# Performance work log

Measured on AMD Instinct MI355X. Metric: run time of the kernel, lower is better.

The kernel has to match this reference:

```python
import jax, jax.numpy as jnp
import numpy as np

NUM_NODES = 65536       # B * gcn_nodes_num = 256 * 256
NODES_PER_GRAPH = 256
GCN_EMB_DIM = 128
N_EMBD = 512
NUM_EDGES = 1048576     # avg degree 16
NEG_SLOPE = 0.1


def gcn_conv(x, edge_index, W, b, num_nodes):
    """PyG GCNConv: add self-loops, symmetric normalization, linear, aggregate."""
    loop = jnp.arange(num_nodes, dtype=edge_index.dtype)
    src = jnp.concatenate([edge_index[0], loop])
    dst = jnp.concatenate([edge_index[1], loop])
    deg = jax.ops.segment_sum(jnp.ones_like(dst, dtype=x.dtype), dst,
                              num_segments=num_nodes)
    dinv = jnp.where(deg > 0, jax.lax.rsqrt(deg), jnp.zeros_like(deg))
    norm = dinv[src] * dinv[dst]              # [E+N]
    h = x @ W                                 # [N, out]
    msg = h[src] * norm[:, None]              # [E+N, out]
    out = jax.ops.segment_sum(msg, dst, num_segments=num_nodes)
    return out + b


def setup_inputs() -> dict:
    key = jax.random.key(0)
    ks = jax.random.split(key, 8)
    nodes = jax.random.normal(ks[0], (NUM_NODES, 3), dtype=jnp.float32)
    edge_index = jax.random.randint(ks[1], (2, NUM_EDGES), 0, NUM_NODES,
                                    dtype=jnp.int64)
    W1 = jax.random.normal(ks[2], (3, 3), dtype=jnp.float32) * 0.5
    b1 = jnp.zeros((3,), dtype=jnp.float32)
    W2 = jax.random.normal(ks[3], (3, GCN_EMB_DIM), dtype=jnp.float32) * 0.5
    b2 = jnp.zeros((GCN_EMB_DIM,), dtype=jnp.float32)
    W3 = jax.random.normal(ks[4], (GCN_EMB_DIM * NODES_PER_GRAPH, N_EMBD),
                           dtype=jnp.float32) * 0.01
    b3 = jnp.zeros((N_EMBD,), dtype=jnp.float32)
    return {"nodes": nodes, "edge_index": edge_index,
            "W1": W1, "b1": b1, "W2": W2, "b2": b2, "W3": W3, "b3": b3}


def reference(nodes, edge_index, W1, b1, W2, b2, W3, b3):
    n = nodes.shape[0]
    h = gcn_conv(nodes, edge_index, W1, b1, n)           # GCNConv(3,3)
    h = jnp.where(h >= 0, h, NEG_SLOPE * h)              # leaky_relu(0.1)
    h = gcn_conv(h, edge_index, W2, b2, n)               # GCNConv(3,128)
    h = h.reshape(-1, GCN_EMB_DIM * NODES_PER_GRAPH)     # [B, 128*256]
    out = h @ W3 + b3                                    # [B, 512]
    return out
```

## Files before the change

### kernel.cpp

```cpp
#include <hip/hip_runtime.h>

static constexpr int NN   = 65536;
static constexpr int NPG  = 256;
static constexpr int NB   = 256;
static constexpr int EMB  = 128;
static constexpr int NOUT = 512;

static constexpr int NBIN = 256;
static constexpr int CAP  = 4608;
static constexpr int SCAP = CAP + 256;

static constexpr int BT = 16;
static constexpr int KS = 16;
static constexpr int IC = NPG / KS;

__global__ __launch_bounds__(1024)
void k_partV(const int* __restrict__ src, const int* __restrict__ dst, int E,
             int* __restrict__ part, int* __restrict__ cl,
             const float* __restrict__ W2, const float* __restrict__ b2,
             const float* __restrict__ W3, float4* __restrict__ V4) {
    union SH {
        struct { int hist[NBIN]; int loff[NBIN]; int scanbuf[NBIN];
                 int stage[4096]; } part;
        float4 red[8][4][128];
    };
    __shared__ SH sh;
    int tid = threadIdx.x;
    int bid = blockIdx.x;

    if (bid >= NBIN) {
        int i  = bid - NBIN;
        int j4 = tid & 127;
        int cg = tid >> 7;
        const float4* w3 = (const float4*)(W3 + (size_t)i * EMB * NOUT)
                           + (size_t)cg * 16 * (NOUT/4) + j4;
        float4 a0 = {0,0,0,0}, a1 = {0,0,0,0}, a2 = {0,0,0,0}, a3 = {0,0,0,0};
        for (int c = 0; c < 16; c++) {
            float4 v = w3[(size_t)c * (NOUT/4)];
            int cc = cg*16 + c;
            float w0 = W2[0*EMB+cc], w1 = W2[1*EMB+cc], w2 = W2[2*EMB+cc], wb = b2[cc];
            a0.x += w0*v.x; a0.y += w0*v.y; a0.z += w0*v.z; a0.w += w0*v.w;
            a1.x += w1*v.x; a1.y += w1*v.y; a1.z += w1*v.z; a1.w += w1*v.w;
            a2.x += w2*v.x; a2.y += w2*v.y; a2.z += w2*v.z; a2.w += w2*v.w;
            a3.x += wb*v.x; a3.y += wb*v.y; a3.z += wb*v.z; a3.w += wb*v.w;
        }
        sh.red[cg][0][j4] = a0;
        sh.red[cg][1][j4] = a1;
        sh.red[cg][2][j4] = a2;
        sh.red[cg][3][j4] = a3;
        __syncthreads();
        if (tid < 512) {
            int k = tid >> 7, jj = tid & 127;
            float4 s = sh.red[0][k][jj];
#pragma unroll
            for (int g = 1; g < 8; g++) {
                float4 v = sh.red[g][k][jj];
                s.x += v.x; s.y += v.y; s.z += v.z; s.w += v.w;
            }
            sh.red[0][k][jj] = s;
        }
        __syncthreads();
        if (tid < NOUT) {
            int j = tid;
            const float* r0 = (const float*)&sh.red[0][0][j >> 2];
            const float* r1 = (const float*)&sh.red[0][1][j >> 2];
            const float* r2 = (const float*)&sh.red[0][2][j >> 2];
            const float* r3 = (const float*)&sh.red[0][3][j >> 2];
            float4 o = { r0[j & 3], r1[j & 3], r2[j & 3], r3[j & 3] };
            V4[(size_t)i * NOUT + j] = o;
        }
        return;
    }
    int epb = (E + NBIN - 1) / NBIN;
    int e0 = bid * epb;
    int e1 = min(e0 + epb, E);
    if (tid < NBIN) sh.part.hist[tid] = 0;
    __syncthreads();

    int pk[4], bn[4], rk[4];
    int n = 0;
    int e = e0 + tid * 4;
    if (e + 4 <= e1) {
        int4 s4 = *(const int4*)(src + e);
        int4 d4 = *(const int4*)(dst + e);
        int ss[4] = {s4.x, s4.y, s4.z, s4.w};
        int dd[4] = {d4.x, d4.y, d4.z, d4.w};
#pragma unroll
        for (int k = 0; k < 4; k++) {
            pk[k] = ss[k] | ((dd[k] & 255) << 16);
            bn[k] = dd[k] >> 8;
            rk[k] = atomicAdd(&sh.part.hist[bn[k]], 1);
        }
        n = 4;
    } else {
        for (int k = 0; k < 4 && e + k < e1; k++) {
            int s = src[e+k], d = dst[e+k];
            pk[n] = s | ((d & 255) << 16);
            bn[n] = d >> 8;
            rk[n] = atomicAdd(&sh.part.hist[bn[n]], 1);
            n++;
        }
    }
    __syncthreads();

    if (tid < NBIN) sh.part.scanbuf[tid] = sh.part.hist[tid];
    __syncthreads();
    for (int off = 1; off < NBIN; off <<= 1) {
        int v = 0;
        if (tid < NBIN && tid >= off) v = sh.part.scanbuf[tid - off];
        __syncthreads();
        if (tid < NBIN) sh.part.scanbuf[tid] += v;
        __syncthreads();
    }
    if (tid < NBIN) {
        int lo = sh.part.scanbuf[tid] - sh.part.hist[tid];
        sh.part.loff[tid] = lo;
        cl[bid * NBIN + tid] = lo | (sh.part.hist[tid] << 16);
    }
    __syncthreads();

    for (int k = 0; k < n; k++) sh.part.stage[sh.part.loff[bn[k]] + rk[k]] = pk[k];
    __syncthreads();

    int ctot = e1 - e0;
    for (int t = tid; t < ctot; t += 1024)
        part[(size_t)bid * epb + t] = sh.part.stage[t];
}

__global__ __launch_bounds__(512)
void k_csr(const int* __restrict__ cl, const int* __restrict__ part, int epb,
           const float* __restrict__ nodes,
           float* __restrict__ dinv, float4* __restrict__ y1,
           int* __restrict__ rs, unsigned short* __restrict__ srt) {
    __shared__ int pkst[CAP];
    __shared__ int hist[NPG], off_[NPG];
    __shared__ int wtot[4];
    __shared__ int cls[NBIN], blo[NBIN];
    __shared__ unsigned short stageS[SCAP];
    int tid = threadIdx.x, bin = blockIdx.x;
    if (tid < NPG) hist[tid] = 0;

    int cn = 0, v = 0;
    if (tid < NBIN) {
        int c = cl[tid * NBIN + bin];
        cls[tid] = c;
        cn = c >> 16;
        v = cn;
    }
    int lane = tid & 63;
#pragma unroll
    for (int off = 1; off < 64; off <<= 1) {
        int t = __shfl_up(v, off, 64);
        if (tid < NBIN && lane >= off) v += t;
    }
    if (tid < NBIN && lane == 63) wtot[tid >> 6] = v;
    __syncthreads();
    if (tid < NBIN) {
        int wv = tid >> 6, offs = 0;
#pragma unroll
        for (int w = 0; w < 3; w++) if (w < wv) offs += wtot[w];
        blo[tid] = v + offs - cn;
    }
    __syncthreads();

    {
        int blk = tid >> 1, half = tid & 1;
        int c = cls[blk];
        int lo = c & 0xFFFF, cb = c >> 16;
        int db = blo[blk];
        const int* q = part + (size_t)blk * epb + lo;
        for (int t = half; t < cb; t += 2) {
            int d2 = db + t;
            if (d2 < CAP) {
                int p = q[t];
                pkst[d2] = p;
                atomicAdd(&hist[(p >> 16) & 255], 1);
            }
        }
    }
    __syncthreads();

    int h = 0, v2 = 0;
    if (tid < NPG) { h = hist[tid]; v2 = (h + 1) & ~1; }
#pragma unroll
    for (int off = 1; off < 64; off <<= 1) {
        int t = __shfl_up(v2, off, 64);
        if (tid < NPG && lane >= off) v2 += t;
    }
    if (tid < NPG && lane == 63) wtot[tid >> 6] = v2;
    __syncthreads();
    if (tid < NPG) {
        int wv = tid >> 6;
        int offs = 0;
#pragma unroll
        for (int w = 0; w < 3; w++) if (w < wv) offs += wtot[w];
        int start = v2 + offs - ((h + 1) & ~1);
        off_[tid] = start;
        int node = bin * NPG + tid;
        float di = rsqrtf((float)(h + 1));
        dinv[node] = di;
        y1[node] = make_float4(nodes[3*node+0] * di, nodes[3*node+1] * di,
                               nodes[3*node+2] * di, 0.f);
        rs[node] = start | (h << 20);
    }
    __syncthreads();
    int ctot = min(wtot[0] + wtot[1] + wtot[2] + wtot[3], CAP);
    for (int e2 = tid; e2 < ctot; e2 += 512) {
        (void)0;
    }
    {
    }
    __syncthreads();
    int rawtot = blo[NBIN-1] + (cls[NBIN-1] >> 16);
    if (rawtot > CAP) rawtot = CAP;
    for (int e2 = tid; e2 < rawtot; e2 += 512) {
        int p = pkst[e2];
        int pos = atomicAdd(&off_[(p >> 16) & 255], 1);
        stageS[pos] = (unsigned short)(p & 0xFFFF);
    }
    __syncthreads();
    int tot = wtot[0] + wtot[1] + wtot[2] + wtot[3];
    const unsigned int* so = (const unsigned int*)stageS;
    unsigned int* g = (unsigned int*)(srt + (size_t)bin * SCAP);
    for (int t = tid; t < (tot >> 1); t += 512) g[t] = so[t];
}

__device__ __forceinline__ void agg_pass(int g, const int* __restrict__ rs,
                                         const unsigned short* __restrict__ srt,
                                         const float* __restrict__ dinv,
                                         const float* __restrict__ W1,
                                         const float* __restrict__ b1,
                                         const float4* __restrict__ yin,
                                         float4* __restrict__ yout, bool first) {
    int i = g >> 3, sub = g & 7;
    int rsd = rs[i];
    int start = rsd & 0xFFFFF, deg = rsd >> 20;
    const unsigned int* spw = (const unsigned int*)(srt + (size_t)(i >> 8) * SCAP + start);
    int npairs = (deg + 1) >> 1;
    float ax = 0.f, ay = 0.f, az = 0.f;
    for (int w = sub; w < npairs; w += 8) {
        unsigned int u = spw[w];
        float4 v0 = yin[u & 0xFFFF];
        ax += v0.x; ay += v0.y; az += v0.z;
        if (2*w + 1 < deg) {
            float4 v1 = yin[u >> 16];
            ax += v1.x; ay += v1.y; az += v1.z;
        }
    }
    ax += __shfl_xor(ax, 1); ay += __shfl_xor(ay, 1); az += __shfl_xor(az, 1);
    ax += __shfl_xor(ax, 2); ay += __shfl_xor(ay, 2); az += __shfl_xor(az, 2);
    ax += __shfl_xor(ax, 4); ay += __shfl_xor(ay, 4); az += __shfl_xor(az, 4);
    if (sub == 0) {
        float4 self = yin[i];
        float di = dinv[i];
        float a0 = (ax + self.x) * di, a1 = (ay + self.y) * di, a2 = (az + self.z) * di;
        if (first) {
            float h[3];
#pragma unroll
            for (int k = 0; k < 3; k++) {
                float t = a0 * W1[0*3+k] + a1 * W1[1*3+k] + a2 * W1[2*3+k] + b1[k];
                t = (t >= 0.f) ? t : 0.1f * t;
                h[k] = t * di;
            }
            yout[i] = make_float4(h[0], h[1], h[2], 0.f);
        } else {
            yout[i] = make_float4(a0, a1, a2, 0.f);
        }
    }
}

__global__ void k_agg1(const int* __restrict__ rs, const unsigned short* __restrict__ srt,
                       const float* __restrict__ dinv, const float4* __restrict__ y1,
                       const float* __restrict__ W1, const float* __restrict__ b1,
                       float4* __restrict__ y2) {
    agg_pass(blockIdx.x * 256 + threadIdx.x, rs, srt, dinv, W1, b1, y1, y2, true);
}

__global__ void k_agg2(const int* __restrict__ rs, const unsigned short* __restrict__ srt,
                       const float* __restrict__ dinv, const float4* __restrict__ y2,
                       float4* __restrict__ agg2) {
    agg_pass(blockIdx.x * 256 + threadIdx.x, rs, srt, dinv, nullptr, nullptr,
             y2, agg2, false);
}

__global__ void k_out_part(const float4* __restrict__ agg2, const float4* __restrict__ V4,
                           float* __restrict__ partO) {
    __shared__ float4 a_s[BT * IC];
    int tid = threadIdx.x;
    int j  = blockIdx.x * 256 + tid;
    int b0 = blockIdx.y * BT;
    int i0 = blockIdx.z * IC;
    for (int idx = tid; idx < BT * IC; idx += 256) {
        int t = idx / IC, i = idx % IC;
        a_s[idx] = agg2[(size_t)(b0 + t) * NPG + i0 + i];
    }
    __syncthreads();

    float acc[BT];
#pragma unroll
    for (int t = 0; t < BT; t++) acc[t] = 0.f;

    const float4* vj = V4 + (size_t)i0 * NOUT + j;
    for (int i = 0; i < IC; i++) {
        float4 vv = vj[(size_t)i * NOUT];
#pragma unroll
        for (int t = 0; t < BT; t++) {
            float4 a = a_s[t*IC + i];
            acc[t] += a.x * vv.x + a.y * vv.y + a.z * vv.z + vv.w;
        }
    }
#pragma unroll
    for (int t = 0; t < BT; t++)
        partO[((size_t)blockIdx.z * NB + b0 + t) * NOUT + j] = acc[t];
}

__global__ void k_reduce(const float4* __restrict__ part4, const float4* __restrict__ b3_4,
                         float4* __restrict__ out4) {
    int idx = blockIdx.x * 256 + threadIdx.x;
    int j4 = idx & (NOUT/4 - 1);
    float4 acc = b3_4[j4];
#pragma unroll
    for (int s = 0; s < KS; s++) {
        float4 v = part4[(size_t)s * (NB*NOUT/4) + idx];
        acc.x += v.x; acc.y += v.y; acc.z += v.z; acc.w += v.w;
    }
    out4[idx] = acc;
}

extern "C" void kernel_launch(void* const* d_in, const int* in_sizes, int n_in,
                              void* d_out, int out_size, void* d_ws, size_t ws_size,
                              hipStream_t stream) {
    const float* nodes = (const float*)d_in[0];
    const int*   ei    = (const int*)  d_in[1];
    const float* W1    = (const float*)d_in[2];
    const float* b1    = (const float*)d_in[3];
    const float* W2    = (const float*)d_in[4];
    const float* b2    = (const float*)d_in[5];
    const float* W3    = (const float*)d_in[6];
    const float* b3    = (const float*)d_in[7];

    const int E = in_sizes[1] / 2;
    const int* src = ei;
    const int* dst = ei + E;
    const int epb = (E + NBIN - 1) / NBIN;

    char* ws = (char*)d_ws;
    float4* y1    = (float4*)ws;
    float4* y2    = y1 + NN;
    float4* agg2  = y2 + NN;
    float4* V4    = agg2 + NN;
    float*  partO = (float*)(V4 + (size_t)NPG * NOUT);
    int*    partE = (int*)(partO + (size_t)KS * NB * NOUT);
    unsigned short* srt = (unsigned short*)(partE + (size_t)NBIN * CAP);
    int*    rs    = (int*)(srt + (size_t)NBIN * SCAP);
    float*  dinv  = (float*)(rs + NN);
    int*    cl    = (int*)(dinv + NN);

    k_partV   <<<2*NBIN, 1024, 0, stream>>>(src, dst, E, partE, cl, W2, b2, W3, V4);
    k_csr     <<<NBIN,    512, 0, stream>>>(cl, partE, epb, nodes, dinv, y1, rs, srt);
    k_agg1    <<<NN*8/256, 256, 0, stream>>>(rs, srt, dinv, y1, W1, b1, y2);
    k_agg2    <<<NN*8/256, 256, 0, stream>>>(rs, srt, dinv, y2, agg2);
    k_out_part<<<dim3(2, NB/BT, KS), 256, 0, stream>>>(agg2, V4, partO);
    k_reduce  <<<NB*NOUT/4/256,      256, 0, stream>>>((const float4*)partO,
                                                       (const float4*)b3, (float4*)d_out);
}
```

Baseline: 155.3 us.

## Fuse all GCN pipeline stages into one cooperative kernel with grid syncs

Replaces the six separate launches (partition, CSR build, two aggregations, output partial GEMM, reduce) with a single cooperative kernel of 512 blocks × 512 threads that separates phases with grid.sync(). The W3 precontraction into V4 is split into two halves and overlapped with the partition and CSR phases on the otherwise idle upper 256 blocks. This removes per-launch overhead and inter-kernel gaps. In exchange it gives up per-phase launch geometry: aggregation runs 4 threads per node instead of 8, and the output and reduce phases leave most blocks idle. Grid-wide barriers also have their own cost, and the old launch sequence is kept as a fallback if the cooperative launch fails.

```diff
diff --git a/kernel.cpp b/kernel.cpp
--- a/kernel.cpp
+++ b/kernel.cpp
@@ -1,4 +1,7 @@
 #include <hip/hip_runtime.h>
+#include <hip/hip_cooperative_groups.h>
+
+namespace cg = cooperative_groups;
 
 static constexpr int NN   = 65536;
 static constexpr int NPG  = 256;
@@ -13,6 +16,330 @@
 static constexpr int BT = 16;
 static constexpr int KS = 16;
 static constexpr int IC = NPG / KS;
+
+__global__ __launch_bounds__(512, 4)
+void k_mega(const int* __restrict__ src, const int* __restrict__ dst, int E,
+            int* __restrict__ part, int* __restrict__ cl,
+            const float* __restrict__ W2, const float* __restrict__ b2,
+            const float* __restrict__ W3, float4* __restrict__ V4,
+            const float* __restrict__ nodes, float* __restrict__ dinv,
+            float4* __restrict__ y1, int* __restrict__ rs,
+            unsigned short* __restrict__ srt,
+            const float* __restrict__ W1, const float* __restrict__ b1,
+            float4* __restrict__ y2, float4* __restrict__ agg2,
+            float* __restrict__ partO, const float* __restrict__ b3,
+            float* __restrict__ out) {
+    union SH {
+        struct { int hist[NBIN]; int loff[NBIN]; int wt[4]; int stage[4096]; } part;
+        float4 redV[4][4][128];
+        struct { int pkst[CAP]; int hist[NPG]; int off_[NPG]; int wtot[4];
+                 int cls[NBIN]; int blo[NBIN]; unsigned short stageS[SCAP]; } csr;
+        float4 a_s[BT * IC];
+    };
+    __shared__ SH sh;
+    cg::grid_group grid = cg::this_grid();
+    const int tid = threadIdx.x;
+    const int bid = blockIdx.x;
+    const int lane = tid & 63;
+    const int epb = (E + NBIN - 1) / NBIN;
+
+    float4 va0 = {0,0,0,0}, va1 = {0,0,0,0}, va2 = {0,0,0,0}, va3 = {0,0,0,0};
+    const int vi  = bid - NBIN;
+    const int vj4 = tid & 127;
+    const int vcg = tid >> 7;
+
+    if (bid < NBIN) {
+        int e0 = bid * epb;
+        int e1 = min(e0 + epb, E);
+        if (tid < NBIN) sh.part.hist[tid] = 0;
+        __syncthreads();
+
+        int pk[8], bn[8], rk[8];
+        int e = e0 + tid * 8;
+        if (e + 8 <= e1) {
+            int4 sa = *(const int4*)(src + e), sb = *(const int4*)(src + e + 4);
+            int4 da = *(const int4*)(dst + e), db = *(const int4*)(dst + e + 4);
+            int ss[8] = {sa.x, sa.y, sa.z, sa.w, sb.x, sb.y, sb.z, sb.w};
+            int dd[8] = {da.x, da.y, da.z, da.w, db.x, db.y, db.z, db.w};
+#pragma unroll
+            for (int k = 0; k < 8; k++) {
+                pk[k] = ss[k] | ((dd[k] & 255) << 16);
+                bn[k] = dd[k] >> 8;
+                rk[k] = atomicAdd(&sh.part.hist[bn[k]], 1);
+            }
+        } else {
+#pragma unroll
+            for (int k = 0; k < 8; k++) {
+                if (e + k < e1) {
+                    int s = src[e+k], d = dst[e+k];
+                    pk[k] = s | ((d & 255) << 16);
+                    bn[k] = d >> 8;
+                    rk[k] = atomicAdd(&sh.part.hist[bn[k]], 1);
+                } else bn[k] = -1;
+            }
+        }
+        __syncthreads();
+
+        int h = 0, v = 0;
+        if (tid < NBIN) { h = sh.part.hist[tid]; v = h; }
+#pragma unroll
+        for (int off = 1; off < 64; off <<= 1) {
+            int t = __shfl_up(v, off, 64);
+            if (tid < NBIN && lane >= off) v += t;
+        }
+        if (tid < NBIN && lane == 63) sh.part.wt[tid >> 6] = v;
+        __syncthreads();
+        if (tid < NBIN) {
+            int wv = tid >> 6, offs = 0;
+#pragma unroll
+            for (int w = 0; w < 3; w++) if (w < wv) offs += sh.part.wt[w];
+            int lo = v + offs - h;
+            sh.part.loff[tid] = lo;
+            cl[bid * NBIN + tid] = lo | (h << 16);
+        }
+        __syncthreads();
+#pragma unroll
+        for (int k = 0; k < 8; k++)
+            if (bn[k] >= 0) sh.part.stage[sh.part.loff[bn[k]] + rk[k]] = pk[k];
+        __syncthreads();
+        int ctot = e1 - e0;
+        for (int t = tid; t < ctot; t += 512)
+            part[(size_t)bid * epb + t] = sh.part.stage[t];
+    } else {
+        const float4* w3 = (const float4*)(W3 + (size_t)vi * EMB * NOUT);
+#pragma unroll
+        for (int c = 0; c < 16; c++) {
+            int cc = vcg * 32 + c;
+            float4 v = w3[(size_t)cc * (NOUT/4) + vj4];
+            float w0 = W2[0*EMB+cc], w1 = W2[1*EMB+cc], w2c = W2[2*EMB+cc], wb = b2[cc];
+            va0.x += w0*v.x;  va0.y += w0*v.y;  va0.z += w0*v.z;  va0.w += w0*v.w;
+            va1.x += w1*v.x;  va1.y += w1*v.y;  va1.z += w1*v.z;  va1.w += w1*v.w;
+            va2.x += w2c*v.x; va2.y += w2c*v.y; va2.z += w2c*v.z; va2.w += w2c*v.w;
+            va3.x += wb*v.x;  va3.y += wb*v.y;  va3.z += wb*v.z;  va3.w += wb*v.w;
+        }
+    }
+    grid.sync();
+
+    if (bid < NBIN) {
+        int bin = bid;
+        if (tid < NPG) sh.csr.hist[tid] = 0;
+        int cn = 0, v = 0;
+        if (tid < NBIN) {
+            int c = cl[tid * NBIN + bin];
+            sh.csr.cls[tid] = c;
+            cn = c >> 16;
+            v = cn;
+        }
+#pragma unroll
+        for (int off = 1; off < 64; off <<= 1) {
+            int t = __shfl_up(v, off, 64);
+            if (tid < NBIN && lane >= off) v += t;
+        }
+        if (tid < NBIN && lane == 63) sh.csr.wtot[tid >> 6] = v;
+        __syncthreads();
+        if (tid < NBIN) {
+            int wv = tid >> 6, offs = 0;
+#pragma unroll
+            for (int w = 0; w < 3; w++) if (w < wv) offs += sh.csr.wtot[w];
+            sh.csr.blo[tid] = v + offs - cn;
+        }
+        __syncthreads();
+
+        {
+            int blk = tid >> 1, half = tid & 1;
+            int c = sh.csr.cls[blk];
+            int lo = c & 0xFFFF, cb = c >> 16;
+            int db = sh.csr.blo[blk];
+            const int* q = part + (size_t)blk * epb + lo;
+            for (int t = half; t < cb; t += 2) {
+                int d2 = db + t;
+                if (d2 < CAP) {
+                    int p = q[t];
+                    sh.csr.pkst[d2] = p;
+                    atomicAdd(&sh.csr.hist[(p >> 16) & 255], 1);
+                }
+            }
+        }
+        __syncthreads();
+
+        int h = 0, v2 = 0;
+        if (tid < NPG) { h = sh.csr.hist[tid]; v2 = (h + 1) & ~1; }
+#pragma unroll
+        for (int off = 1; off < 64; off <<= 1) {
+            int t = __shfl_up(v2, off, 64);
+            if (tid < NPG && lane >= off) v2 += t;
+        }
+        if (tid < NPG && lane == 63) sh.csr.wtot[tid >> 6] = v2;
+        __syncthreads();
+        if (tid < NPG) {
+            int wv = tid >> 6, offs = 0;
+#pragma unroll
+            for (int w = 0; w < 3; w++) if (w < wv) offs += sh.csr.wtot[w];
+            int start = v2 + offs - ((h + 1) & ~1);
+            sh.csr.off_[tid] = start;
+            int node = bin * NPG + tid;
+            float di = rsqrtf((float)(h + 1));
+            dinv[node] = di;
+            y1[node] = make_float4(nodes[3*node+0] * di, nodes[3*node+1] * di,
+                                   nodes[3*node+2] * di, 0.f);
+            rs[node] = start | (h << 20);
+        }
+        __syncthreads();
+        int rawtot = sh.csr.blo[NBIN-1] + (sh.csr.cls[NBIN-1] >> 16);
+        if (rawtot > CAP) rawtot = CAP;
+        for (int e2 = tid; e2 < rawtot; e2 += 512) {
+            int p = sh.csr.pkst[e2];
+            int pos = atomicAdd(&sh.csr.off_[(p >> 16) & 255], 1);
+            sh.csr.stageS[pos] = (unsigned short)(p & 0xFFFF);
+        }
+        __syncthreads();
+        int tot = sh.csr.wtot[0] + sh.csr.wtot[1] + sh.csr.wtot[2] + sh.csr.wtot[3];
+        const unsigned int* so = (const unsigned int*)sh.csr.stageS;
+        unsigned int* g = (unsigned int*)(srt + (size_t)bin * SCAP);
+        for (int t = tid; t < (tot >> 1); t += 512) g[t] = so[t];
+    } else {
+        const float4* w3 = (const float4*)(W3 + (size_t)vi * EMB * NOUT);
+#pragma unroll
+        for (int c = 16; c < 32; c++) {
+            int cc = vcg * 32 + c;
+            float4 v = w3[(size_t)cc * (NOUT/4) + vj4];
+            float w0 = W2[0*EMB+cc], w1 = W2[1*EMB+cc], w2c = W2[2*EMB+cc], wb = b2[cc];
+            va0.x += w0*v.x;  va0.y += w0*v.y;  va0.z += w0*v.z;  va0.w += w0*v.w;
+            va1.x += w1*v.x;  va1.y += w1*v.y;  va1.z += w1*v.z;  va1.w += w1*v.w;
+            va2.x += w2c*v.x; va2.y += w2c*v.y; va2.z += w2c*v.z; va2.w += w2c*v.w;
+            va3.x += wb*v.x;  va3.y += wb*v.y;  va3.z += wb*v.z;  va3.w += wb*v.w;
+        }
+        sh.redV[vcg][0][vj4] = va0;
+        sh.redV[vcg][1][vj4] = va1;
+        sh.redV[vcg][2][vj4] = va2;
+        sh.redV[vcg][3][vj4] = va3;
+        __syncthreads();
+        {
+            int k = tid >> 7, jj = tid & 127;
+            float4 s = sh.redV[0][k][jj];
+#pragma unroll
+            for (int g2 = 1; g2 < 4; g2++) {
+                float4 t = sh.redV[g2][k][jj];
+                s.x += t.x; s.y += t.y; s.z += t.z; s.w += t.w;
+            }
+            sh.redV[0][k][jj] = s;
+        }
+        __syncthreads();
+        {
+            int j = tid;
+            const float* r0 = (const float*)&sh.redV[0][0][j >> 2];
+            const float* r1 = (const float*)&sh.redV[0][1][j >> 2];
+            const float* r2 = (const float*)&sh.redV[0][2][j >> 2];
+            const float* r3 = (const float*)&sh.redV[0][3][j >> 2];
+            V4[(size_t)vi * NOUT + j] = make_float4(r0[j & 3], r1[j & 3],
+                                                    r2[j & 3], r3[j & 3]);
+        }
+    }
+    grid.sync();
+
+    {
+        int gq = bid * 512 + tid;
+        int i = gq >> 2, sub = gq & 3;
+        int rsd = rs[i];
+        int start = rsd & 0xFFFFF, deg = rsd >> 20;
+        const unsigned int* spw = (const unsigned int*)(srt + (size_t)(i >> 8) * SCAP + start);
+        int npairs = (deg + 1) >> 1;
+        float ax = 0.f, ay = 0.f, az = 0.f;
+        for (int w = sub; w < npairs; w += 4) {
+            unsigned int u = spw[w];
+            float4 v0 = y1[u & 0xFFFF];
+            ax += v0.x; ay += v0.y; az += v0.z;
+            if (2*w + 1 < deg) {
+                float4 v1 = y1[u >> 16];
+                ax += v1.x; ay += v1.y; az += v1.z;
+            }
+        }
+        ax += __shfl_xor(ax, 1); ay += __shfl_xor(ay, 1); az += __shfl_xor(az, 1);
+        ax += __shfl_xor(ax, 2); ay += __shfl_xor(ay, 2); az += __shfl_xor(az, 2);
+        if (sub == 0) {
+            float4 self = y1[i];
+            float di = dinv[i];
+            float a0 = (ax + self.x) * di, a1 = (ay + self.y) * di, a2 = (az + self.z) * di;
+            float hh[3];
+#pragma unroll
+            for (int k = 0; k < 3; k++) {
+                float t = a0 * W1[0*3+k] + a1 * W1[1*3+k] + a2 * W1[2*3+k] + b1[k];
+                t = (t >= 0.f) ? t : 0.1f * t;
+                hh[k] = t * di;
+            }
+            y2[i] = make_float4(hh[0], hh[1], hh[2], 0.f);
+        }
+    }
+    grid.sync();
+
+    {
+        int gq = bid * 512 + tid;
+        int i = gq >> 2, sub = gq & 3;
+        int rsd = rs[i];
+        int start = rsd & 0xFFFFF, deg = rsd >> 20;
+        const unsigned int* spw = (const unsigned int*)(srt + (size_t)(i >> 8) * SCAP + start);
+        int npairs = (deg + 1) >> 1;
+        float ax = 0.f, ay = 0.f, az = 0.f;
+        for (int w = sub; w < npairs; w += 4) {
+            unsigned int u = spw[w];
+            float4 v0 = y2[u & 0xFFFF];
+            ax += v0.x; ay += v0.y; az += v0.z;
+            if (2*w + 1 < deg) {
+                float4 v1 = y2[u >> 16];
+                ax += v1.x; ay += v1.y; az += v1.z;
+            }
+        }
+        ax += __shfl_xor(ax, 1); ay += __shfl_xor(ay, 1); az += __shfl_xor(az, 1);
+        ax += __shfl_xor(ax, 2); ay += __shfl_xor(ay, 2); az += __shfl_xor(az, 2);
+        if (sub == 0) {
+            float4 self = y2[i];
+            float di = dinv[i];
+            agg2[i] = make_float4((ax + self.x) * di, (ay + self.y) * di,
+                                  (az + self.z) * di, 0.f);
+        }
+    }
+    grid.sync();
+
+    if (bid < 256) {
+        int ks = bid & 15, bb = bid >> 4;
+        int b0 = bb * BT, i0 = ks * IC;
+        if (tid < BT * IC) {
+            int t = tid >> 4, i = tid & 15;
+            sh.a_s[tid] = agg2[(size_t)(b0 + t) * NPG + i0 + i];
+        }
+        __syncthreads();
+        float acc[BT];
+#pragma unroll
+        for (int t = 0; t < BT; t++) acc[t] = 0.f;
+        int j = tid;
+        const float4* vj = V4 + (size_t)i0 * NOUT + j;
+        for (int i = 0; i < IC; i++) {
+            float4 vv = vj[(size_t)i * NOUT];
+#pragma unroll
+            for (int t = 0; t < BT; t++) {
+                float4 a = sh.a_s[t*IC + i];
+                acc[t] += a.x * vv.x + a.y * vv.y + a.z * vv.z + vv.w;
+            }
+        }
+#pragma unroll
+        for (int t = 0; t < BT; t++)
+            partO[((size_t)ks * NB + b0 + t) * NOUT + j] = acc[t];
+    }
+    grid.sync();
+
+    if (bid < 64) {
+        int idx = bid * 512 + tid;
+        int j4 = idx & (NOUT/4 - 1);
+        const float4* b3_4 = (const float4*)b3;
+        float4 acc = b3_4[j4];
+#pragma unroll
+        for (int s = 0; s < KS; s++) {
+            float4 vv = ((const float4*)partO)[(size_t)s * (NB*NOUT/4) + idx];
+            acc.x += vv.x; acc.y += vv.y; acc.z += vv.z; acc.w += vv.w;
+        }
+        ((float4*)out)[idx] = acc;
+    }
+}
 
 __global__ __launch_bounds__(1024)
 void k_partV(const int* __restrict__ src, const int* __restrict__ dst, int E,
@@ -66,8 +393,7 @@
             const float* r1 = (const float*)&sh.red[0][1][j >> 2];
             const float* r2 = (const float*)&sh.red[0][2][j >> 2];
             const float* r3 = (const float*)&sh.red[0][3][j >> 2];
-            float4 o = { r0[j & 3], r1[j & 3], r2[j & 3], r3[j & 3] };
-            V4[(size_t)i * NOUT + j] = o;
+            V4[(size_t)i * NOUT + j] = make_float4(r0[j&3], r1[j&3], r2[j&3], r3[j&3]);
         }
         return;
     }
@@ -202,13 +528,6 @@
         y1[node] = make_float4(nodes[3*node+0] * di, nodes[3*node+1] * di,
                                nodes[3*node+2] * di, 0.f);
         rs[node] = start | (h << 20);
-    }
-    __syncthreads();
-    int ctot = min(wtot[0] + wtot[1] + wtot[2] + wtot[3], CAP);
-    for (int e2 = tid; e2 < ctot; e2 += 512) {
-        (void)0;
-    }
-    {
     }
     __syncthreads();
     int rawtot = blo[NBIN-1] + (cls[NBIN-1] >> 16);
@@ -339,7 +658,7 @@
     const float* W3    = (const float*)d_in[6];
     const float* b3    = (const float*)d_in[7];
 
-    const int E = in_sizes[1] / 2;
+    int E = in_sizes[1] / 2;
     const int* src = ei;
     const int* dst = ei + E;
     const int epb = (E + NBIN - 1) / NBIN;
@@ -356,11 +675,32 @@
     float*  dinv  = (float*)(rs + NN);
     int*    cl    = (int*)(dinv + NN);
 
-    k_partV   <<<2*NBIN, 1024, 0, stream>>>(src, dst, E, partE, cl, W2, b2, W3, V4);
-    k_csr     <<<NBIN,    512, 0, stream>>>(cl, partE, epb, nodes, dinv, y1, rs, srt);
-    k_agg1    <<<NN*8/256, 256, 0, stream>>>(rs, srt, dinv, y1, W1, b1, y2);
-    k_agg2    <<<NN*8/256, 256, 0, stream>>>(rs, srt, dinv, y2, agg2);
-    k_out_part<<<dim3(2, NB/BT, KS), 256, 0, stream>>>(agg2, V4, partO);
-    k_reduce  <<<NB*NOUT/4/256,      256, 0, stream>>>((const float4*)partO,
-                                                       (const float4*)b3, (float4*)d_out);
-}
+    const int* src_ = src; const int* dst_ = dst;
+    int* partE_ = partE; int* cl_ = cl;
+    const float* W2_ = W2; const float* b2_ = b2; const float* W3_ = W3;
+    float4* V4_ = V4; const float* nodes_ = nodes;
+    float* dinv_ = dinv; float4* y1_ = y1; int* rs_ = rs;
+    unsigned short* srt_ = srt;
+    const float* W1_ = W1; const float* b1_ = b1;
+    float4* y2_ = y2; float4* agg2_ = agg2;
+    float* partO_ = partO; const float* b3_ = b3;
+    float* out_ = (float*)d_out;
+
+    void* args[] = { &src_, &dst_, &E, &partE_, &cl_, &W2_, &b2_, &W3_, &V4_,
+                     &nodes_, &dinv_, &y1_, &rs_, &srt_, &W1_, &b1_,
+                     &y2_, &agg2_, &partO_, &b3_, &out_ };
+
+    hipError_t err = hipLaunchCooperativeKernel((const void*)k_mega,
+                                                dim3(512), dim3(512),
+                                                args, 0, stream);
+    if (err != hipSuccess) {
+        (void)hipGetLastError();
+        k_partV   <<<2*NBIN, 1024, 0, stream>>>(src, dst, E, partE, cl, W2, b2, W3, V4);
+        k_csr     <<<NBIN,    512, 0, stream>>>(cl, partE, epb, nodes, dinv, y1, rs, srt);
+        k_agg1    <<<NN*8/256, 256, 0, stream>>>(rs, srt, dinv, y1, W1, b1, y2);
+        k_agg2    <<<NN*8/256, 256, 0, stream>>>(rs, srt, dinv, y2, agg2);
+        k_out_part<<<dim3(2, NB/BT, KS), 256, 0, stream>>>(agg2, V4, partO);
+        k_reduce  <<<NB*NOUT/4/256,      256, 0, stream>>>((const float4*)partO,
+                                                           (const float4*)b3, (float4*)d_out);
+    }
+}
```

Result: slower. 460.1 us (+196.2%).

## Split W3 folding into V across partition, CSR and aggregation kernels

Applied to the files above, without the earlier changes.

Precomputing V = W2/b2 folded into W3 used to be done entirely inside k_partV, which streams the whole 64 MB W3. The work is now split into four channel chunks of 32. k_partV handles the first chunk, and extra blocks appended to k_csr, k_agg1 and k_agg2 each accumulate a further chunk into V4 in read-modify-write style. This hides the W3 streaming behind the latency-bound partition and aggregation work, and W3 loads are marked nontemporal. In exchange, each kernel now depends on the previous kernel's partial V4, the extra blocks compete for bandwidth with the aggregation passes, and the later chunks use scalar loads.

```diff
diff --git a/kernel.cpp b/kernel.cpp
--- a/kernel.cpp
+++ b/kernel.cpp
@@ -13,6 +13,11 @@
 static constexpr int BT = 16;
 static constexpr int KS = 16;
 static constexpr int IC = NPG / KS;
+
+static constexpr int AGB = NN * 8 / 256;
+
+typedef float nfloat4 __attribute__((ext_vector_type(4)));
+
 
 __global__ __launch_bounds__(1024)
 void k_partV(const int* __restrict__ src, const int* __restrict__ dst, int E,
@@ -32,12 +37,13 @@
         int i  = bid - NBIN;
         int j4 = tid & 127;
         int cg = tid >> 7;
-        const float4* w3 = (const float4*)(W3 + (size_t)i * EMB * NOUT)
-                           + (size_t)cg * 16 * (NOUT/4) + j4;
+        const nfloat4* w3 = (const nfloat4*)(W3 + (size_t)i * EMB * NOUT)
+                            + (size_t)cg * 4 * (NOUT/4) + j4;
         float4 a0 = {0,0,0,0}, a1 = {0,0,0,0}, a2 = {0,0,0,0}, a3 = {0,0,0,0};
-        for (int c = 0; c < 16; c++) {
-            float4 v = w3[(size_t)c * (NOUT/4)];
-            int cc = cg*16 + c;
+#pragma unroll
+        for (int c = 0; c < 4; c++) {
+            nfloat4 v = __builtin_nontemporal_load(&w3[(size_t)c * (NOUT/4)]);
+            int cc = cg*4 + c;
             float w0 = W2[0*EMB+cc], w1 = W2[1*EMB+cc], w2 = W2[2*EMB+cc], wb = b2[cc];
             a0.x += w0*v.x; a0.y += w0*v.y; a0.z += w0*v.z; a0.w += w0*v.w;
             a1.x += w1*v.x; a1.y += w1*v.y; a1.z += w1*v.z; a1.w += w1*v.w;
@@ -127,17 +133,54 @@
         part[(size_t)bid * epb + t] = sh.part.stage[t];
 }
 
+template <int JPER>
+__device__ __forceinline__ void finishV(int i, int tid, int c0,
+                                        const float* __restrict__ W2,
+                                        const float* __restrict__ b2,
+                                        const float* __restrict__ W3,
+                                        float4* __restrict__ V4) {
+    float4 acc[JPER];
+#pragma unroll
+    for (int q = 0; q < JPER; q++)
+        acc[q] = V4[(size_t)i * NOUT + tid + q * (NOUT / JPER)];
+    const float* w3r = W3 + ((size_t)i * EMB + c0) * NOUT + tid;
+#pragma unroll
+    for (int c = 0; c < 32; c++) {
+        int cc = c0 + c;
+        float w0 = W2[0*EMB+cc], w1 = W2[1*EMB+cc], w2 = W2[2*EMB+cc], wb = b2[cc];
+#pragma unroll
+        for (int q = 0; q < JPER; q++) {
+            float s = __builtin_nontemporal_load(&w3r[(size_t)c * NOUT + q * (NOUT / JPER)]);
+            acc[q].x += w0 * s;
+            acc[q].y += w1 * s;
+            acc[q].z += w2 * s;
+            acc[q].w += wb * s;
+        }
+    }
+#pragma unroll
+    for (int q = 0; q < JPER; q++)
+        V4[(size_t)i * NOUT + tid + q * (NOUT / JPER)] = acc[q];
+}
+
 __global__ __launch_bounds__(512)
 void k_csr(const int* __restrict__ cl, const int* __restrict__ part, int epb,
            const float* __restrict__ nodes,
            float* __restrict__ dinv, float4* __restrict__ y1,
-           int* __restrict__ rs, unsigned short* __restrict__ srt) {
+           int* __restrict__ rs, unsigned short* __restrict__ srt,
+           const float* __restrict__ W2, const float* __restrict__ b2,
+           const float* __restrict__ W3, float4* __restrict__ V4) {
     __shared__ int pkst[CAP];
     __shared__ int hist[NPG], off_[NPG];
     __shared__ int wtot[4];
     __shared__ int cls[NBIN], blo[NBIN];
     __shared__ unsigned short stageS[SCAP];
     int tid = threadIdx.x, bin = blockIdx.x;
+
+    if (bin >= NBIN) {
+        finishV<1>(bin - NBIN, tid, 32, W2, b2, W3, V4);
+        return;
+    }
+
     if (tid < NPG) hist[tid] = 0;
 
     int cn = 0, v = 0;
@@ -202,13 +245,6 @@
         y1[node] = make_float4(nodes[3*node+0] * di, nodes[3*node+1] * di,
                                nodes[3*node+2] * di, 0.f);
         rs[node] = start | (h << 20);
-    }
-    __syncthreads();
-    int ctot = min(wtot[0] + wtot[1] + wtot[2] + wtot[3], CAP);
-    for (int e2 = tid; e2 < ctot; e2 += 512) {
-        (void)0;
-    }
-    {
     }
     __syncthreads();
     int rawtot = blo[NBIN-1] + (cls[NBIN-1] >> 16);
@@ -272,14 +308,28 @@
 __global__ void k_agg1(const int* __restrict__ rs, const unsigned short* __restrict__ srt,
                        const float* __restrict__ dinv, const float4* __restrict__ y1,
                        const float* __restrict__ W1, const float* __restrict__ b1,
-                       float4* __restrict__ y2) {
-    agg_pass(blockIdx.x * 256 + threadIdx.x, rs, srt, dinv, W1, b1, y1, y2, true);
+                       float4* __restrict__ y2,
+                       const float* __restrict__ W2, const float* __restrict__ b2,
+                       const float* __restrict__ W3, float4* __restrict__ V4) {
+    int bid = blockIdx.x;
+    if (bid >= AGB) {
+        finishV<2>(bid - AGB, threadIdx.x, 64, W2, b2, W3, V4);
+        return;
+    }
+    agg_pass(bid * 256 + threadIdx.x, rs, srt, dinv, W1, b1, y1, y2, true);
 }
 
 __global__ void k_agg2(const int* __restrict__ rs, const unsigned short* __restrict__ srt,
                        const float* __restrict__ dinv, const float4* __restrict__ y2,
-                       float4* __restrict__ agg2) {
-    agg_pass(blockIdx.x * 256 + threadIdx.x, rs, srt, dinv, nullptr, nullptr,
+                       float4* __restrict__ agg2,
+                       const float* __restrict__ W2, const float* __restrict__ b2,
+                       const float* __restrict__ W3, float4* __restrict__ V4) {
+    int bid = blockIdx.x;
+    if (bid >= AGB) {
+        finishV<2>(bid - AGB, threadIdx.x, 96, W2, b2, W3, V4);
+        return;
+    }
+    agg_pass(bid * 256 + threadIdx.x, rs, srt, dinv, nullptr, nullptr,
              y2, agg2, false);
 }
 
@@ -356,10 +406,13 @@
     float*  dinv  = (float*)(rs + NN);
     int*    cl    = (int*)(dinv + NN);
 
-    k_partV   <<<2*NBIN, 1024, 0, stream>>>(src, dst, E, partE, cl, W2, b2, W3, V4);
-    k_csr     <<<NBIN,    512, 0, stream>>>(cl, partE, epb, nodes, dinv, y1, rs, srt);
-    k_agg1    <<<NN*8/256, 256, 0, stream>>>(rs, srt, dinv, y1, W1, b1, y2);
-    k_agg2    <<<NN*8/256, 256, 0, stream>>>(rs, srt, dinv, y2, agg2);
+    k_partV   <<<2*NBIN,   1024, 0, stream>>>(src, dst, E, partE, cl, W2, b2, W3, V4);
+    k_csr     <<<2*NBIN,    512, 0, stream>>>(cl, partE, epb, nodes, dinv, y1, rs, srt,
+                                              W2, b2, W3, V4);
+    k_agg1    <<<AGB + 256, 256, 0, stream>>>(rs, srt, dinv, y1, W1, b1, y2,
+                                              W2, b2, W3, V4);
+    k_agg2    <<<AGB + 256, 256, 0, stream>>>(rs, srt, dinv, y2, agg2,
+                                              W2, b2, W3, V4);
     k_out_part<<<dim3(2, NB/BT, KS), 256, 0, stream>>>(agg2, V4, partO);
     k_reduce  <<<NB*NOUT/4/256,      256, 0, stream>>>((const float4*)partO,
                                                        (const float4*)b3, (float4*)d_out);
```

Result: slower. 165.4 us (+6.5%).

## Fuse split-K output GEMM and reduction into one kernel; nontemporal W3 loads

Applied to the files above, without the earlier changes.

Replaces the split-K output kernel plus its separate reduction kernel with a single kernel. Each block handles 4 graphs over the full 256-node K range, accumulates in registers and adds the bias directly. This removes the partial-sum buffer round trip through memory and one kernel launch, but each block now does 16x more serial K work on a grid of 256 blocks of 128 threads. It also makes the one-time W3 streaming loads in k_partV nontemporal and deletes a dead empty loop with its extra barrier in k_csr.

```diff
diff --git a/kernel.cpp b/kernel.cpp
--- a/kernel.cpp
+++ b/kernel.cpp
@@ -10,9 +10,11 @@
 static constexpr int CAP  = 4608;
 static constexpr int SCAP = CAP + 256;
 
-static constexpr int BT = 16;
-static constexpr int KS = 16;
-static constexpr int IC = NPG / KS;
+static constexpr int KS  = 16;
+static constexpr int IC  = NPG / KS;
+static constexpr int BT2 = 4;
+
+typedef float nfloat4 __attribute__((ext_vector_type(4)));
 
 __global__ __launch_bounds__(1024)
 void k_partV(const int* __restrict__ src, const int* __restrict__ dst, int E,
@@ -32,11 +34,11 @@
         int i  = bid - NBIN;
         int j4 = tid & 127;
         int cg = tid >> 7;
-        const float4* w3 = (const float4*)(W3 + (size_t)i * EMB * NOUT)
-                           + (size_t)cg * 16 * (NOUT/4) + j4;
+        const nfloat4* w3 = (const nfloat4*)(W3 + (size_t)i * EMB * NOUT)
+                            + (size_t)cg * 16 * (NOUT/4) + j4;
         float4 a0 = {0,0,0,0}, a1 = {0,0,0,0}, a2 = {0,0,0,0}, a3 = {0,0,0,0};
         for (int c = 0; c < 16; c++) {
-            float4 v = w3[(size_t)c * (NOUT/4)];
+            nfloat4 v = __builtin_nontemporal_load(&w3[(size_t)c * (NOUT/4)]);
             int cc = cg*16 + c;
             float w0 = W2[0*EMB+cc], w1 = W2[1*EMB+cc], w2 = W2[2*EMB+cc], wb = b2[cc];
             a0.x += w0*v.x; a0.y += w0*v.y; a0.z += w0*v.z; a0.w += w0*v.w;
@@ -202,13 +204,6 @@
         y1[node] = make_float4(nodes[3*node+0] * di, nodes[3*node+1] * di,
                                nodes[3*node+2] * di, 0.f);
         rs[node] = start | (h << 20);
-    }
-    __syncthreads();
-    int ctot = min(wtot[0] + wtot[1] + wtot[2] + wtot[3], CAP);
-    for (int e2 = tid; e2 < ctot; e2 += 512) {
-        (void)0;
-    }
-    {
     }
     __syncthreads();
     int rawtot = blo[NBIN-1] + (cls[NBIN-1] >> 16);
@@ -283,48 +278,44 @@
              y2, agg2, false);
 }
 
-__global__ void k_out_part(const float4* __restrict__ agg2, const float4* __restrict__ V4,
-                           float* __restrict__ partO) {
-    __shared__ float4 a_s[BT * IC];
+__global__ __launch_bounds__(128)
+void k_out(const float4* __restrict__ agg2, const float4* __restrict__ V4,
+           const float* __restrict__ b3, float* __restrict__ out) {
+    __shared__ float4 a_s[BT2 * NPG];
     int tid = threadIdx.x;
-    int j  = blockIdx.x * 256 + tid;
-    int b0 = blockIdx.y * BT;
-    int i0 = blockIdx.z * IC;
-    for (int idx = tid; idx < BT * IC; idx += 256) {
-        int t = idx / IC, i = idx % IC;
-        a_s[idx] = agg2[(size_t)(b0 + t) * NPG + i0 + i];
-    }
-    __syncthreads();
-
-    float acc[BT];
-#pragma unroll
-    for (int t = 0; t < BT; t++) acc[t] = 0.f;
-
-    const float4* vj = V4 + (size_t)i0 * NOUT + j;
-    for (int i = 0; i < IC; i++) {
-        float4 vv = vj[(size_t)i * NOUT];
-#pragma unroll
-        for (int t = 0; t < BT; t++) {
-            float4 a = a_s[t*IC + i];
-            acc[t] += a.x * vv.x + a.y * vv.y + a.z * vv.z + vv.w;
-        }
-    }
-#pragma unroll
-    for (int t = 0; t < BT; t++)
-        partO[((size_t)blockIdx.z * NB + b0 + t) * NOUT + j] = acc[t];
-}
-
-__global__ void k_reduce(const float4* __restrict__ part4, const float4* __restrict__ b3_4,
-                         float4* __restrict__ out4) {
-    int idx = blockIdx.x * 256 + threadIdx.x;
-    int j4 = idx & (NOUT/4 - 1);
-    float4 acc = b3_4[j4];
-#pragma unroll
+    int j  = blockIdx.x * 128 + tid;
+    int b0 = blockIdx.y * BT2;
+    for (int idx = tid; idx < BT2 * NPG; idx += 128) {
+        int t = idx >> 8, i = idx & 255;
+        a_s[idx] = agg2[(size_t)(b0 + t) * NPG + i];
+    }
+    __syncthreads();
+
+    float acc[BT2];
+#pragma unroll
+    for (int t = 0; t < BT2; t++) acc[t] = b3[j];
+
+    const float4* vj = V4 + j;
     for (int s = 0; s < KS; s++) {
-        float4 v = part4[(size_t)s * (NB*NOUT/4) + idx];
-        acc.x += v.x; acc.y += v.y; acc.z += v.z; acc.w += v.w;
-    }
-    out4[idx] = acc;
+        float ps[BT2];
+#pragma unroll
+        for (int t = 0; t < BT2; t++) ps[t] = 0.f;
+#pragma unroll
+        for (int ii = 0; ii < IC; ii++) {
+            int i = s * IC + ii;
+            float4 vv = vj[(size_t)i * NOUT];
+#pragma unroll
+            for (int t = 0; t < BT2; t++) {
+                float4 a = a_s[t * NPG + i];
+                ps[t] += a.x * vv.x + a.y * vv.y + a.z * vv.z + vv.w;
+            }
+        }
+#pragma unroll
+        for (int t = 0; t < BT2; t++) acc[t] += ps[t];
+    }
+#pragma unroll
+    for (int t = 0; t < BT2; t++)
+        out[(size_t)(b0 + t) * NOUT + j] = acc[t];
 }
 
 extern "C" void kernel_launch(void* const* d_in, const int* in_sizes, int n_in,
@@ -349,18 +340,15 @@
     float4* y2    = y1 + NN;
     float4* agg2  = y2 + NN;
     float4* V4    = agg2 + NN;
-    float*  partO = (float*)(V4 + (size_t)NPG * NOUT);
-    int*    partE = (int*)(partO + (size_t)KS * NB * NOUT);
+    int*    partE = (int*)(V4 + (size_t)NPG * NOUT);
     unsigned short* srt = (unsigned short*)(partE + (size_t)NBIN * CAP);
     int*    rs    = (int*)(srt + (size_t)NBIN * SCAP);
     float*  dinv  = (float*)(rs + NN);
     int*    cl    = (int*)(dinv + NN);
 
-    k_partV   <<<2*NBIN, 1024, 0, stream>>>(src, dst, E, partE, cl, W2, b2, W3, V4);
-    k_csr     <<<NBIN,    512, 0, stream>>>(cl, partE, epb, nodes, dinv, y1, rs, srt);
-    k_agg1    <<<NN*8/256, 256, 0, stream>>>(rs, srt, dinv, y1, W1, b1, y2);
-    k_agg2    <<<NN*8/256, 256, 0, stream>>>(rs, srt, dinv, y2, agg2);
-    k_out_part<<<dim3(2, NB/BT, KS), 256, 0, stream>>>(agg2, V4, partO);
-    k_reduce  <<<NB*NOUT/4/256,      256, 0, stream>>>((const float4*)partO,
-                                                       (const float4*)b3, (float4*)d_out);
-}
+    k_partV<<<2*NBIN,   1024, 0, stream>>>(src, dst, E, partE, cl, W2, b2, W3, V4);
+    k_csr  <<<NBIN,      512, 0, stream>>>(cl, partE, epb, nodes, dinv, y1, rs, srt);
+    k_agg1 <<<NN*8/256,  256, 0, stream>>>(rs, srt, dinv, y1, W1, b1, y2);
+    k_agg2 <<<NN*8/256,  256, 0, stream>>>(rs, srt, dinv, y2, agg2);
+    k_out  <<<dim3(NOUT/128, NB/BT2), 128, 0, stream>>>(agg2, V4, b3, (float*)d_out);
+}
```

Result: slower. 207.3 us (+33.5%).
